# Kernel tuning notes

Measured on AMD Instinct MI355X. Metric: run time of the kernel, lower is better.

Reference implementation:

```python
import jax, jax.numpy as jnp
import numpy as np

B, S, D, H = 2, 2048, 4096, 16
HD = D // H          # 256 head dim
ROT = 64             # rotary_dim
MASK_FILL = -65504.0 # fp16 min, as in the IPEX kernel


def _sinusoidal_positions(num_pos, dim):
    inv_freq = 1.0 / (10000.0 ** (np.arange(0, dim, 2, dtype=np.float32) / dim))
    sinusoid = np.einsum('i,j->ij', np.arange(num_pos, dtype=np.float32), inv_freq)
    return np.concatenate([np.sin(sinusoid), np.cos(sinusoid)], axis=-1).astype(np.float32)  # [num_pos, dim]


def setup_inputs() -> dict:
    key = jax.random.key(0)
    ks = jax.random.split(key, 6)
    w = 0.02
    return {
        'hidden_states': jax.random.normal(ks[0], (B, S, D), jnp.float32),
        'Wq': jax.random.normal(ks[1], (D, D), jnp.float32) * w,
        'Wk': jax.random.normal(ks[2], (D, D), jnp.float32) * w,
        'Wv': jax.random.normal(ks[3], (D, D), jnp.float32) * w,
        'Wo': jax.random.normal(ks[4], (D, D), jnp.float32) * w,
        'embed_positions': jnp.asarray(_sinusoidal_positions(S, ROT)),  # [max_pos, ROT] sin|cos
        'attention_mask': jnp.zeros((B, 1, 1, S), jnp.float32),
        'position_ids': jnp.tile(jnp.arange(S, dtype=jnp.int32), (B, 1)),
    }


def rotate_every_two(x):
    x1 = x[..., ::2]
    x2 = x[..., 1::2]
    return jnp.stack((-x2, x1), axis=-1).reshape(x.shape)


def reference(hidden_states, Wq, Wk, Wv, Wo, embed_positions, attention_mask, position_ids):
    b, s, d = hidden_states.shape
    q = (hidden_states @ Wq).reshape(b, s, H, HD)
    k = (hidden_states @ Wk).reshape(b, s, H, HD)
    v = (hidden_states @ Wv).reshape(b, s, H, HD)

    # gather sin/cos per position, GPT-J interleaved layout
    sincos = embed_positions[position_ids]            # [b, s, ROT]
    sin, cos = jnp.split(sincos, 2, axis=-1)          # each [b, s, ROT/2]
    sin = jnp.repeat(sin, 2, axis=-1)[:, :, None, :]  # [b, s, 1, ROT]
    cos = jnp.repeat(cos, 2, axis=-1)[:, :, None, :]

    def rope(t):
        tr = t[..., :ROT]
        tr = tr * cos + rotate_every_two(tr) * sin
        return jnp.concatenate([tr, t[..., ROT:]], axis=-1)

    q = rope(q).transpose(0, 2, 1, 3)  # [b, H, s, HD]
    k = rope(k).transpose(0, 2, 1, 3)
    v = v.transpose(0, 2, 1, 3)

    scores = jnp.einsum('bhqd,bhkd->bhqk', q, k)
    causal = jnp.tril(jnp.ones((s, s), bool))
    # IPEX order: mask-fill with -65504 BEFORE dividing by sqrt(head_dim)
    scores = jnp.where(causal, scores, MASK_FILL) / jnp.sqrt(jnp.float32(HD))
    scores = scores + attention_mask
    attn = jax.nn.softmax(scores, axis=-1)

    out = jnp.einsum('bhqk,bhkd->bhqd', attn, v)
    out = out.transpose(0, 2, 1, 3).reshape(b, s, d)
    return out @ Wo
```

## Files before the change

kernel.cpp:

```cpp
#include <hip/hip_runtime.h>

typedef __bf16 bf16x8 __attribute__((ext_vector_type(8)));
typedef float f32x4 __attribute__((ext_vector_type(4)));
typedef unsigned short u16;
typedef unsigned int u32;
typedef u16 u16x8 __attribute__((ext_vector_type(8)));
typedef u16 u16x4 __attribute__((ext_vector_type(4)));

#define DEVI __device__ __forceinline__

static constexpr size_t R_ELEMS = (size_t)4096 * 4096;

DEVI u16 f2bf(float f) {
  u32 x = __float_as_uint(f);
  u32 r = x + 0x7FFFu + ((x >> 16) & 1u);
  return (u16)(r >> 16);
}
DEVI float bf2f(u16 u) { return __uint_as_float(((u32)u) << 16); }

#define GLOAD_LDS16(gp, lp)                                                     \
  __builtin_amdgcn_global_load_lds(                                             \
      (const __attribute__((address_space(1))) void*)(gp),                      \
      (__attribute__((address_space(3))) void*)(lp), 16, 0, 0)

__global__ void k_cvt(const float* __restrict__ in, u16* __restrict__ out, int n8) {
  int i = blockIdx.x * blockDim.x + threadIdx.x;
  if (i >= n8) return;
  const float4* p = (const float4*)in + (size_t)i * 2;
  float4 a = p[0], b = p[1];
  u16x8 o;
  o[0] = f2bf(a.x); o[1] = f2bf(a.y); o[2] = f2bf(a.z); o[3] = f2bf(a.w);
  o[4] = f2bf(b.x); o[5] = f2bf(b.y); o[6] = f2bf(b.z); o[7] = f2bf(b.w);
  *((u16x8*)out + i) = o;
}

__global__ void k_transpose_w(const float* __restrict__ W, u16* __restrict__ Wt) {
  __shared__ float t[64][65];
  int kb = blockIdx.x * 64, nb = blockIdx.y * 64;
  int tx = threadIdx.x, ty = threadIdx.y;
#pragma unroll
  for (int i = 0; i < 16; i++) {
    int r = i * 4 + ty;
    t[r][tx] = W[(size_t)(kb + r) * 4096 + nb + tx];
  }
  __syncthreads();
#pragma unroll
  for (int i = 0; i < 16; i++) {
    int r = i * 4 + ty;
    Wt[(size_t)(nb + r) * 4096 + kb + tx] = f2bf(t[tx][r]);
  }
}

__global__ void k_transpose_v(const u16* __restrict__ V, u16* __restrict__ Vt) {
  __shared__ u16 t[64][65];
  int s0 = blockIdx.x * 64, d0 = blockIdx.y * 64;
  size_t base = (size_t)blockIdx.z * (2048 * 256);
  int tx = threadIdx.x, ty = threadIdx.y;
#pragma unroll
  for (int i = 0; i < 16; i++) {
    int r = i * 4 + ty;
    t[r][tx] = V[base + (size_t)(s0 + r) * 256 + d0 + tx];
  }
  __syncthreads();
#pragma unroll
  for (int i = 0; i < 16; i++) {
    int r = i * 4 + ty;
    Vt[base + (size_t)(d0 + r) * 2048 + s0 + tx] = t[tx][r];
  }
}

__global__ void k_rope(u16* __restrict__ q, u16* __restrict__ k,
                       const float* __restrict__ ep, const int* __restrict__ pid) {
  int gid = blockIdx.x * blockDim.x + threadIdx.x;
  int pair = gid & 31;
  int row = gid >> 5;
  u16* base = (row < 65536) ? q : k;
  int rr = row & 65535;
  int b = rr >> 15;
  int s = rr & 2047;
  int pos = pid[b * 2048 + s];
  float sn = ep[pos * 64 + pair];
  float cs = ep[pos * 64 + 32 + pair];
  u16* p = base + (size_t)rr * 256 + pair * 2;
  float x0 = bf2f(p[0]), x1 = bf2f(p[1]);
  p[0] = f2bf(x0 * cs - x1 * sn);
  p[1] = f2bf(x1 * cs + x0 * sn);
}

template <int OUTMODE>
__global__ __launch_bounds__(256, 2) void k_gemm(const u16* __restrict__ A,
                                                 const u16* __restrict__ Bt,
                                                 void* __restrict__ outp) {
  __shared__ __attribute__((aligned(16))) u16 lA[128 * 64];
  __shared__ __attribute__((aligned(16))) u16 lB[128 * 64];
  const int tid = threadIdx.x;
  const int w = tid >> 6, lane = tid & 63;
  const int wr = w >> 1, wc = w & 1;
  const int m0 = blockIdx.y * 128, n0 = blockIdx.x * 128;

  f32x4 acc[4][4];
#pragma unroll
  for (int i = 0; i < 4; i++)
#pragma unroll
    for (int j = 0; j < 4; j++) acc[i][j] = (f32x4){0.f, 0.f, 0.f, 0.f};

  const int srow = lane >> 3;
  const int scol = ((lane & 7) ^ srow) * 8;
  const u16* Abase = A + (size_t)(m0 + w * 32 + srow) * 4096 + scol;
  const u16* Bbase = Bt + (size_t)(n0 + w * 32 + srow) * 4096 + scol;
  u16* lAw = lA + w * 2048;
  u16* lBw = lB + w * 2048;

  const int lm = lane & 15;
  const int lk = lane >> 4;
  const int swz = (lane & 7) << 3;

  for (int kt = 0; kt < 64; ++kt) {
    __syncthreads();
#pragma unroll
    for (int i = 0; i < 4; ++i) {
      GLOAD_LDS16(Abase + (size_t)kt * 64 + (size_t)i * 8 * 4096, lAw + i * 512);
      GLOAD_LDS16(Bbase + (size_t)kt * 64 + (size_t)i * 8 * 4096, lBw + i * 512);
    }
    __syncthreads();
#pragma unroll
    for (int ks = 0; ks < 2; ++ks) {
      bf16x8 af[4], bfr[4];
      const int ce = (ks * 32 + lk * 8) ^ swz;
#pragma unroll
      for (int mi = 0; mi < 4; mi++)
        af[mi] = *(const bf16x8*)(lA + (wr * 64 + mi * 16 + lm) * 64 + ce);
#pragma unroll
      for (int ni = 0; ni < 4; ni++)
        bfr[ni] = *(const bf16x8*)(lB + (wc * 64 + ni * 16 + lm) * 64 + ce);
#pragma unroll
      for (int mi = 0; mi < 4; mi++)
#pragma unroll
        for (int ni = 0; ni < 4; ni++)
          acc[mi][ni] = __builtin_amdgcn_mfma_f32_16x16x32_bf16(af[mi], bfr[ni],
                                                                acc[mi][ni], 0, 0, 0);
    }
  }

#pragma unroll
  for (int mi = 0; mi < 4; mi++) {
#pragma unroll
    for (int ni = 0; ni < 4; ni++) {
#pragma unroll
      for (int r = 0; r < 4; r++) {
        int m = m0 + wr * 64 + mi * 16 + lk * 4 + r;
        int n = n0 + wc * 64 + ni * 16 + lm;
        float v = acc[mi][ni][r];
        if (OUTMODE == 0) {
          u16* o = (u16*)outp;
          o[(size_t)((m >> 11) * 16 + (n >> 8)) * 524288 + (size_t)(m & 2047) * 256 +
            (n & 255)] = f2bf(v);
        } else {
          float* o = (float*)outp;
          o[(size_t)m * 4096 + n] = v;
        }
      }
    }
  }
}

__global__ __launch_bounds__(512, 2) void k_attn(const u16* __restrict__ Q,
                                                 const u16* __restrict__ K,
                                                 const u16* __restrict__ Vt,
                                                 const float* __restrict__ amask,
                                                 u16* __restrict__ AO) {
  __shared__ __attribute__((aligned(16))) u16 lK[2][64 * 256];
  __shared__ __attribute__((aligned(16))) u16 lV[2][256 * 64];
  __shared__ __attribute__((aligned(16))) u16 lP[8][16 * 64];

  const int tid = threadIdx.x, w = tid >> 6, lane = tid & 63;
  const int wg = blockIdx.x;
  const int bh = wg & 31;
  const int qt = (wg < 256) ? (15 - (wg >> 5)) : ((wg - 256) >> 5);
  const int b = bh >> 4;
  const int lm = lane & 15, lk = lane >> 4;
  const size_t head = (size_t)bh * (2048 * 256);
  const int q0 = qt * 128 + w * 16;
  const int swzl = (lane & 7) << 3;

  const int kreg_row = (lane >> 5);
  const int kcol = (lane & 31) * 8;
  const int vreg_row = (lane >> 3);
  const int vcol = (lane & 7) * 8;

#define ASTAGE(t)                                                                \
  {                                                                              \
    const int bb_ = (t) & 1;                                                     \
    const int kv0_ = (t) * 64;                                                   \
    _Pragma("unroll") for (int i_ = 0; i_ < 4; i_++) {                           \
      const int reg_ = w + i_ * 8;                                               \
      const int krow_ = reg_ * 2 + kreg_row;                                     \
      GLOAD_LDS16(K + head + (size_t)(kv0_ + krow_) * 256 +                      \
                      (kcol ^ ((krow_ & 7) << 3)),                               \
                  &lK[bb_][reg_ * 512 + lane * 8]);                              \
      const int vrow_ = reg_ * 8 + vreg_row;                                     \
      GLOAD_LDS16(Vt + head + (size_t)vrow_ * 2048 + kv0_ +                      \
                      (vcol ^ ((vrow_ & 7) << 3)),                               \
                  &lV[bb_][reg_ * 512 + lane * 8]);                              \
    }                                                                            \
  }

  bf16x8 qf[8];
#pragma unroll
  for (int c = 0; c < 8; c++)
    qf[c] = *(const bf16x8*)(Q + head + (size_t)(q0 + lm) * 256 + c * 32 + lk * 8);

  f32x4 o[16];
#pragma unroll
  for (int i = 0; i < 16; i++) o[i] = (f32x4){0.f, 0.f, 0.f, 0.f};
  float m_s = -__builtin_inff();
  float l_s = 0.f;

  const int ntiles = 2 * qt + 2;
  ASTAGE(0);

  for (int t = 0; t < ntiles; ++t) {
    const int kv0 = t * 64;
    const int bb = t & 1;
    float4 amq[4];
#pragma unroll
    for (int kb = 0; kb < 4; kb++)
      amq[kb] = *(const float4*)(amask + b * 2048 + kv0 + kb * 16 + lk * 4);
    if (t + 1 < ntiles) {
      ASTAGE(t + 1);
      asm volatile("s_waitcnt vmcnt(8)" ::: "memory");
    } else {
      asm volatile("s_waitcnt vmcnt(0)" ::: "memory");
    }
    __builtin_amdgcn_s_barrier();

    if (q0 + 15 >= kv0) {
      const u16* lKb = lK[bb];
      const u16* lVb = lV[bb];

      float sx[4][4];
      __builtin_amdgcn_s_setprio(1);
#pragma unroll
      for (int kb = 0; kb < 4; kb++) {
        f32x4 sa = (f32x4){0.f, 0.f, 0.f, 0.f};
        const int kvr = kb * 16 + lm;
#pragma unroll
        for (int c = 0; c < 8; c++) {
          bf16x8 kf = *(const bf16x8*)(lKb + kvr * 256 + ((c * 32 + lk * 8) ^ swzl));
          sa = __builtin_amdgcn_mfma_f32_16x16x32_bf16(kf, qf[c], sa, 0, 0, 0);
        }
#pragma unroll
        for (int r = 0; r < 4; r++)
          sx[kb][r] = sa[r] * 0.0625f + ((const float*)&amq[kb])[r];
      }
      __builtin_amdgcn_s_setprio(0);

      const int q_abs = q0 + lm;
      float tm = -__builtin_inff();
#pragma unroll
      for (int kb = 0; kb < 4; kb++)
#pragma unroll
        for (int r = 0; r < 4; r++) {
          bool valid = (kv0 + kb * 16 + lk * 4 + r) <= q_abs;
          tm = fmaxf(tm, valid ? sx[kb][r] : -__builtin_inff());
        }
      tm = fmaxf(tm, __shfl_xor(tm, 16, 64));
      tm = fmaxf(tm, __shfl_xor(tm, 32, 64));

      if (!__all(tm <= m_s + 8.0f)) {
        float mnew = fmaxf(m_s, tm);
        float alpha = __expf(m_s - mnew);
        m_s = mnew;
        l_s *= alpha;
        float af0 = __shfl(alpha, lk * 4 + 0, 64);
        float af1 = __shfl(alpha, lk * 4 + 1, 64);
        float af2 = __shfl(alpha, lk * 4 + 2, 64);
        float af3 = __shfl(alpha, lk * 4 + 3, 64);
#pragma unroll
        for (int dblk = 0; dblk < 16; dblk++) {
          o[dblk][0] *= af0; o[dblk][1] *= af1;
          o[dblk][2] *= af2; o[dblk][3] *= af3;
        }
      }

      float psum = 0.f;
#pragma unroll
      for (int kb = 0; kb < 4; kb++) {
        u16x4 ph;
#pragma unroll
        for (int r = 0; r < 4; r++) {
          bool valid = (kv0 + kb * 16 + lk * 4 + r) <= q_abs;
          float p = valid ? __expf(sx[kb][r] - m_s) : 0.f;
          psum += p;
          ph[r] = f2bf(p);
        }
        *(u16x4*)(&lP[w][lm * 64 + ((kb * 16 + lk * 4) ^ swzl)]) = ph;
      }
      psum += __shfl_xor(psum, 16, 64);
      psum += __shfl_xor(psum, 32, 64);
      l_s += psum;

      bf16x8 pa[2];
#pragma unroll
      for (int kh = 0; kh < 2; kh++)
        pa[kh] = *(const bf16x8*)(&lP[w][lm * 64 + ((lk * 8 + kh * 32) ^ swzl)]);
      __builtin_amdgcn_s_setprio(1);
#pragma unroll
      for (int dblk = 0; dblk < 16; dblk++) {
        const int dr = dblk * 16 + lm;
#pragma unroll
        for (int kh = 0; kh < 2; kh++) {
          bf16x8 vf = *(const bf16x8*)(lVb + dr * 64 + ((lk * 8 + kh * 32) ^ swzl));
          o[dblk] = __builtin_amdgcn_mfma_f32_16x16x32_bf16(pa[kh], vf, o[dblk], 0, 0, 0);
        }
      }
      __builtin_amdgcn_s_setprio(0);
    }
    __builtin_amdgcn_s_barrier();
  }
#undef ASTAGE

  float linv[4];
#pragma unroll
  for (int r = 0; r < 4; r++) linv[r] = 1.0f / __shfl(l_s, lk * 4 + r, 64);
#pragma unroll
  for (int r = 0; r < 4; r++) {
    const int s_abs = q0 + lk * 4 + r;
#pragma unroll
    for (int dblk = 0; dblk < 16; dblk++) {
      int d = (bh & 15) * 256 + dblk * 16 + lm;
      AO[((size_t)b * 2048 + s_abs) * 4096 + d] = f2bf(o[dblk][r] * linv[r]);
    }
  }
}

extern "C" void kernel_launch(void* const* d_in, const int* in_sizes, int n_in,
                              void* d_out, int out_size, void* d_ws, size_t ws_size,
                              hipStream_t stream) {
  (void)in_sizes; (void)n_in; (void)out_size; (void)ws_size;
  const float* hs = (const float*)d_in[0];
  const float* Wq = (const float*)d_in[1];
  const float* Wk = (const float*)d_in[2];
  const float* Wv = (const float*)d_in[3];
  const float* Wo = (const float*)d_in[4];
  const float* ep = (const float*)d_in[5];
  const float* am = (const float*)d_in[6];
  const int* pid = (const int*)d_in[7];

  u16* r0 = (u16*)d_ws;
  u16* r1 = r0 + R_ELEMS;
  u16* r2 = r1 + R_ELEMS;
  u16* r3 = r2 + R_ELEMS;
  u16* r4 = r3 + R_ELEMS;
  float* out = (float*)d_out;

  dim3 b256(256), b512(512), bT(64, 4);
  k_cvt<<<dim3(8192), b256, 0, stream>>>(hs, r0, 16777216 / 8);

  k_transpose_w<<<dim3(64, 64), bT, 0, stream>>>(Wq, r1);
  k_gemm<0><<<dim3(32, 32), b256, 0, stream>>>(r0, r1, r2);
  k_transpose_w<<<dim3(64, 64), bT, 0, stream>>>(Wk, r1);
  k_gemm<0><<<dim3(32, 32), b256, 0, stream>>>(r0, r1, r3);
  k_transpose_w<<<dim3(64, 64), bT, 0, stream>>>(Wv, r1);
  k_gemm<0><<<dim3(32, 32), b256, 0, stream>>>(r0, r1, r4);

  k_rope<<<dim3(16384), b256, 0, stream>>>(r2, r3, ep, pid);
  k_transpose_v<<<dim3(32, 4, 32), bT, 0, stream>>>(r4, r0);

  k_attn<<<dim3(512), b512, 0, stream>>>(r2, r3, r0, am, r4);

  k_transpose_w<<<dim3(64, 64), bT, 0, stream>>>(Wo, r1);
  k_gemm<1><<<dim3(32, 32), b256, 0, stream>>>(r4, r1, out);
}
```

Measured before the change: 776.3 us.

## Rewrite GEMM as 256x256 tile, 8-wave, double-buffered LDS pipeline with XCD remap

The bf16 GEMM goes from a 128x128 tile with 4 waves and a single LDS buffer to a 256x256 tile with 8 waves. Global-to-LDS loads are double-buffered and interleaved into four MFMA phases, using explicit vmcnt waits, barriers and setprio. Block IDs are remapped so neighbouring tiles land on the same XCD for better L2 reuse. The aim is to hide load latency behind MFMA work and raise data reuse, at the cost of 128KB of LDS, more registers, and a grid of only 256 blocks, which gives one wave of work with possible tail imbalance.

```diff
diff --git a/kernel.cpp b/kernel.cpp
--- a/kernel.cpp
+++ b/kernel.cpp
@@ -22,6 +22,8 @@
   __builtin_amdgcn_global_load_lds(                                             \
       (const __attribute__((address_space(1))) void*)(gp),                      \
       (__attribute__((address_space(3))) void*)(lp), 16, 0, 0)
+
+#define MFMA16(a, b, c) __builtin_amdgcn_mfma_f32_16x16x32_bf16((a), (b), (c), 0, 0, 0)
 
 __global__ void k_cvt(const float* __restrict__ in, u16* __restrict__ out, int n8) {
   int i = blockIdx.x * blockDim.x + threadIdx.x;
@@ -88,68 +90,148 @@
 }
 
 template <int OUTMODE>
-__global__ __launch_bounds__(256, 2) void k_gemm(const u16* __restrict__ A,
+__global__ __launch_bounds__(512, 2) void k_gemm(const u16* __restrict__ A,
                                                  const u16* __restrict__ Bt,
                                                  void* __restrict__ outp) {
-  __shared__ __attribute__((aligned(16))) u16 lA[128 * 64];
-  __shared__ __attribute__((aligned(16))) u16 lB[128 * 64];
+  __shared__ __attribute__((aligned(16))) u16 lA[2][256 * 64];
+  __shared__ __attribute__((aligned(16))) u16 lB[2][256 * 64];
   const int tid = threadIdx.x;
-  const int w = tid >> 6, lane = tid & 63;
-  const int wr = w >> 1, wc = w & 1;
-  const int m0 = blockIdx.y * 128, n0 = blockIdx.x * 128;
-
-  f32x4 acc[4][4];
-#pragma unroll
-  for (int i = 0; i < 4; i++)
+  const int w = tid >> 6, l = tid & 63;
+  const int wm = w >> 2, wn = w & 3;
+  const int bid = blockIdx.x;
+  const int wg = (bid & 7) * 32 + (bid >> 3);
+  const int m0 = (wg >> 4) * 256, n0 = (wg & 15) * 256;
+
+  const int lm = l & 15, lk = l >> 4;
+  const int co0 = (lk ^ (l & 7)) * 8;
+  const int co1 = ((4 + lk) ^ (l & 7)) * 8;
+
+  const int srow = w * 16 + (l >> 3);
+  const int scol = ((l & 7) ^ ((l >> 3) & 7)) * 8;
+  const int ldoff = w * 1024 + l * 8;
+
+  f32x4 acc[8][4];
+#pragma unroll
+  for (int i = 0; i < 8; i++)
 #pragma unroll
     for (int j = 0; j < 4; j++) acc[i][j] = (f32x4){0.f, 0.f, 0.f, 0.f};
 
-  const int srow = lane >> 3;
-  const int scol = ((lane & 7) ^ srow) * 8;
-  const u16* Abase = A + (size_t)(m0 + w * 32 + srow) * 4096 + scol;
-  const u16* Bbase = Bt + (size_t)(n0 + w * 32 + srow) * 4096 + scol;
-  u16* lAw = lA + w * 2048;
-  u16* lBw = lB + w * 2048;
-
-  const int lm = lane & 15;
-  const int lk = lane >> 4;
-  const int swz = (lane & 7) << 3;
-
-  for (int kt = 0; kt < 64; ++kt) {
-    __syncthreads();
-#pragma unroll
-    for (int i = 0; i < 4; ++i) {
-      GLOAD_LDS16(Abase + (size_t)kt * 64 + (size_t)i * 8 * 4096, lAw + i * 512);
-      GLOAD_LDS16(Bbase + (size_t)kt * 64 + (size_t)i * 8 * 4096, lBw + i * 512);
-    }
-    __syncthreads();
-#pragma unroll
-    for (int ks = 0; ks < 2; ++ks) {
-      bf16x8 af[4], bfr[4];
-      const int ce = (ks * 32 + lk * 8) ^ swz;
-#pragma unroll
-      for (int mi = 0; mi < 4; mi++)
-        af[mi] = *(const bf16x8*)(lA + (wr * 64 + mi * 16 + lm) * 64 + ce);
-#pragma unroll
-      for (int ni = 0; ni < 4; ni++)
-        bfr[ni] = *(const bf16x8*)(lB + (wc * 64 + ni * 16 + lm) * 64 + ce);
-#pragma unroll
-      for (int mi = 0; mi < 4; mi++)
-#pragma unroll
-        for (int ni = 0; ni < 4; ni++)
-          acc[mi][ni] = __builtin_amdgcn_mfma_f32_16x16x32_bf16(af[mi], bfr[ni],
-                                                                acc[mi][ni], 0, 0, 0);
-    }
-  }
-
-#pragma unroll
-  for (int mi = 0; mi < 4; mi++) {
+  auto stage_ht = [&](int h) {
+    if (h >= 256) return;
+    const int kt = h >> 2;
+    const int slot = h & 3;
+    const int rowbase = (slot >> 1) << 7;
+    const size_t gcol = (size_t)kt * 64 + scol;
+    if (slot & 1) {
+      const u16* g = A + (size_t)(m0 + rowbase + srow) * 4096 + gcol;
+      u16* d = &lA[kt & 1][rowbase * 64 + ldoff];
+      GLOAD_LDS16(g, d);
+      GLOAD_LDS16(g + 8 * 4096, d + 512);
+    } else {
+      const u16* g = Bt + (size_t)(n0 + rowbase + srow) * 4096 + gcol;
+      u16* d = &lB[kt & 1][rowbase * 64 + ldoff];
+      GLOAD_LDS16(g, d);
+      GLOAD_LDS16(g + 8 * 4096, d + 512);
+    }
+  };
+
+  for (int h = 0; h < 6; ++h) stage_ht(h);
+  asm volatile("s_waitcnt vmcnt(4)" ::: "memory");
+  __builtin_amdgcn_s_barrier();
+
+  bf16x8 af[4][2], bl[2][2], bh[2][2];
+
+  for (int t = 0; t < 64; ++t) {
+    const int hb = 4 * t + 6;
+    const u16* pA = &lA[t & 1][(wm * 128 + lm) * 64];
+    const u16* pB = &lB[t & 1][(wn * 64 + lm) * 64];
+
+#pragma unroll
+    for (int mi = 0; mi < 4; ++mi) {
+      af[mi][0] = *(const bf16x8*)(pA + mi * 1024 + co0);
+      af[mi][1] = *(const bf16x8*)(pA + mi * 1024 + co1);
+    }
+#pragma unroll
+    for (int ni = 0; ni < 2; ++ni) {
+      bl[ni][0] = *(const bf16x8*)(pB + ni * 1024 + co0);
+      bl[ni][1] = *(const bf16x8*)(pB + ni * 1024 + co1);
+    }
+    stage_ht(hb);
+    __builtin_amdgcn_s_barrier();
+    __builtin_amdgcn_s_setprio(1);
+#pragma unroll
+    for (int mi = 0; mi < 4; ++mi)
+#pragma unroll
+      for (int ni = 0; ni < 2; ++ni) {
+        acc[mi][ni] = MFMA16(af[mi][0], bl[ni][0], acc[mi][ni]);
+        acc[mi][ni] = MFMA16(af[mi][1], bl[ni][1], acc[mi][ni]);
+      }
+    __builtin_amdgcn_s_setprio(0);
+    __builtin_amdgcn_s_barrier();
+
+#pragma unroll
+    for (int ni = 0; ni < 2; ++ni) {
+      bh[ni][0] = *(const bf16x8*)(pB + (2 + ni) * 1024 + co0);
+      bh[ni][1] = *(const bf16x8*)(pB + (2 + ni) * 1024 + co1);
+    }
+    stage_ht(hb + 1);
+    __builtin_amdgcn_s_barrier();
+    __builtin_amdgcn_s_setprio(1);
+#pragma unroll
+    for (int mi = 0; mi < 4; ++mi)
+#pragma unroll
+      for (int ni = 0; ni < 2; ++ni) {
+        acc[mi][2 + ni] = MFMA16(af[mi][0], bh[ni][0], acc[mi][2 + ni]);
+        acc[mi][2 + ni] = MFMA16(af[mi][1], bh[ni][1], acc[mi][2 + ni]);
+      }
+    __builtin_amdgcn_s_setprio(0);
+    __builtin_amdgcn_s_barrier();
+
+#pragma unroll
+    for (int mi = 0; mi < 4; ++mi) {
+      af[mi][0] = *(const bf16x8*)(pA + (4 + mi) * 1024 + co0);
+      af[mi][1] = *(const bf16x8*)(pA + (4 + mi) * 1024 + co1);
+    }
+    stage_ht(hb + 2);
+    __builtin_amdgcn_s_barrier();
+    __builtin_amdgcn_s_setprio(1);
+#pragma unroll
+    for (int mi = 0; mi < 4; ++mi)
+#pragma unroll
+      for (int ni = 0; ni < 2; ++ni) {
+        acc[4 + mi][2 + ni] = MFMA16(af[mi][0], bh[ni][0], acc[4 + mi][2 + ni]);
+        acc[4 + mi][2 + ni] = MFMA16(af[mi][1], bh[ni][1], acc[4 + mi][2 + ni]);
+      }
+    __builtin_amdgcn_s_setprio(0);
+    __builtin_amdgcn_s_barrier();
+
+    stage_ht(hb + 3);
+    if (t < 62) {
+      asm volatile("s_waitcnt vmcnt(4)" ::: "memory");
+    } else {
+      asm volatile("s_waitcnt vmcnt(0)" ::: "memory");
+    }
+    __builtin_amdgcn_s_barrier();
+    __builtin_amdgcn_s_setprio(1);
+#pragma unroll
+    for (int mi = 0; mi < 4; ++mi)
+#pragma unroll
+      for (int ni = 0; ni < 2; ++ni) {
+        acc[4 + mi][ni] = MFMA16(af[mi][0], bl[ni][0], acc[4 + mi][ni]);
+        acc[4 + mi][ni] = MFMA16(af[mi][1], bl[ni][1], acc[4 + mi][ni]);
+      }
+    __builtin_amdgcn_s_setprio(0);
+    __builtin_amdgcn_s_barrier();
+  }
+
+#pragma unroll
+  for (int mi = 0; mi < 8; mi++) {
 #pragma unroll
     for (int ni = 0; ni < 4; ni++) {
 #pragma unroll
       for (int r = 0; r < 4; r++) {
-        int m = m0 + wr * 64 + mi * 16 + lk * 4 + r;
-        int n = n0 + wc * 64 + ni * 16 + lm;
+        int m = m0 + wm * 128 + mi * 16 + lk * 4 + r;
+        int n = n0 + wn * 64 + ni * 16 + lm;
         float v = acc[mi][ni][r];
         if (OUTMODE == 0) {
           u16* o = (u16*)outp;
@@ -358,11 +440,11 @@
   k_cvt<<<dim3(8192), b256, 0, stream>>>(hs, r0, 16777216 / 8);
 
   k_transpose_w<<<dim3(64, 64), bT, 0, stream>>>(Wq, r1);
-  k_gemm<0><<<dim3(32, 32), b256, 0, stream>>>(r0, r1, r2);
+  k_gemm<0><<<dim3(256), b512, 0, stream>>>(r0, r1, r2);
   k_transpose_w<<<dim3(64, 64), bT, 0, stream>>>(Wk, r1);
-  k_gemm<0><<<dim3(32, 32), b256, 0, stream>>>(r0, r1, r3);
+  k_gemm<0><<<dim3(256), b512, 0, stream>>>(r0, r1, r3);
   k_transpose_w<<<dim3(64, 64), bT, 0, stream>>>(Wv, r1);
-  k_gemm<0><<<dim3(32, 32), b256, 0, stream>>>(r0, r1, r4);
+  k_gemm<0><<<dim3(256), b512, 0, stream>>>(r0, r1, r4);
 
   k_rope<<<dim3(16384), b256, 0, stream>>>(r2, r3, ep, pid);
   k_transpose_v<<<dim3(32, 4, 32), bT, 0, stream>>>(r4, r0);
@@ -370,5 +452,5 @@
   k_attn<<<dim3(512), b512, 0, stream>>>(r2, r3, r0, am, r4);
 
   k_transpose_w<<<dim3(64, 64), bT, 0, stream>>>(Wo, r1);
-  k_gemm<1><<<dim3(32, 32), b256, 0, stream>>>(r4, r1, out);
-}
+  k_gemm<1><<<dim3(256), b512, 0, stream>>>(r4, r1, out);
+}
```

Result: no change. 783.1 us (+0.9%).

## Fuse Q and K projection GEMMs into one kernel sharing A tiles

Applied to the files above, without the earlier changes.

Adds a k_gemm_qk kernel that computes the Q and K projections together, loading each activation tile into LDS once and multiplying it against both weight tiles. The activation matrix is read from global memory once instead of twice, and one GEMM launch is removed. In exchange each block keeps two accumulator sets (128 fp32 values per lane) and uses 48KB of LDS, which may cause register spills or lower occupancy under launch_bounds(256,2). Workspace buffers are reassigned so that Wk gets its own transposed buffer.

```diff
diff --git a/kernel.cpp b/kernel.cpp
--- a/kernel.cpp
+++ b/kernel.cpp
@@ -22,6 +22,8 @@
   __builtin_amdgcn_global_load_lds(                                             \
       (const __attribute__((address_space(1))) void*)(gp),                      \
       (__attribute__((address_space(3))) void*)(lp), 16, 0, 0)
+
+#define MFMA16(a, b, c) __builtin_amdgcn_mfma_f32_16x16x32_bf16((a), (b), (c), 0, 0, 0)
 
 __global__ void k_cvt(const float* __restrict__ in, u16* __restrict__ out, int n8) {
   int i = blockIdx.x * blockDim.x + threadIdx.x;
@@ -137,8 +139,7 @@
       for (int mi = 0; mi < 4; mi++)
 #pragma unroll
         for (int ni = 0; ni < 4; ni++)
-          acc[mi][ni] = __builtin_amdgcn_mfma_f32_16x16x32_bf16(af[mi], bfr[ni],
-                                                                acc[mi][ni], 0, 0, 0);
+          acc[mi][ni] = MFMA16(af[mi], bfr[ni], acc[mi][ni]);
     }
   }
 
@@ -159,6 +160,93 @@
           float* o = (float*)outp;
           o[(size_t)m * 4096 + n] = v;
         }
+      }
+    }
+  }
+}
+
+__global__ __launch_bounds__(256, 2) void k_gemm_qk(const u16* __restrict__ A,
+                                                    const u16* __restrict__ Btq,
+                                                    const u16* __restrict__ Btk,
+                                                    u16* __restrict__ Qo,
+                                                    u16* __restrict__ Ko) {
+  __shared__ __attribute__((aligned(16))) u16 lA[128 * 64];
+  __shared__ __attribute__((aligned(16))) u16 lBq[128 * 64];
+  __shared__ __attribute__((aligned(16))) u16 lBk[128 * 64];
+  const int tid = threadIdx.x;
+  const int w = tid >> 6, lane = tid & 63;
+  const int wr = w >> 1, wc = w & 1;
+  const int m0 = blockIdx.y * 128, n0 = blockIdx.x * 128;
+
+  f32x4 accq[4][4], acck[4][4];
+#pragma unroll
+  for (int i = 0; i < 4; i++)
+#pragma unroll
+    for (int j = 0; j < 4; j++) {
+      accq[i][j] = (f32x4){0.f, 0.f, 0.f, 0.f};
+      acck[i][j] = (f32x4){0.f, 0.f, 0.f, 0.f};
+    }
+
+  const int srow = lane >> 3;
+  const int scol = ((lane & 7) ^ srow) * 8;
+  const u16* Abase = A + (size_t)(m0 + w * 32 + srow) * 4096 + scol;
+  const u16* Bqb = Btq + (size_t)(n0 + w * 32 + srow) * 4096 + scol;
+  const u16* Bkb = Btk + (size_t)(n0 + w * 32 + srow) * 4096 + scol;
+  u16* lAw = lA + w * 2048;
+  u16* lBqw = lBq + w * 2048;
+  u16* lBkw = lBk + w * 2048;
+
+  const int lm = lane & 15;
+  const int lk = lane >> 4;
+  const int swz = (lane & 7) << 3;
+
+  for (int kt = 0; kt < 64; ++kt) {
+    __syncthreads();
+#pragma unroll
+    for (int i = 0; i < 4; ++i) {
+      GLOAD_LDS16(Abase + (size_t)kt * 64 + (size_t)i * 8 * 4096, lAw + i * 512);
+      GLOAD_LDS16(Bqb + (size_t)kt * 64 + (size_t)i * 8 * 4096, lBqw + i * 512);
+      GLOAD_LDS16(Bkb + (size_t)kt * 64 + (size_t)i * 8 * 4096, lBkw + i * 512);
+    }
+    __syncthreads();
+#pragma unroll
+    for (int ks = 0; ks < 2; ++ks) {
+      bf16x8 af[4], bfr[4];
+      const int ce = (ks * 32 + lk * 8) ^ swz;
+#pragma unroll
+      for (int mi = 0; mi < 4; mi++)
+        af[mi] = *(const bf16x8*)(lA + (wr * 64 + mi * 16 + lm) * 64 + ce);
+#pragma unroll
+      for (int ni = 0; ni < 4; ni++)
+        bfr[ni] = *(const bf16x8*)(lBq + (wc * 64 + ni * 16 + lm) * 64 + ce);
+#pragma unroll
+      for (int mi = 0; mi < 4; mi++)
+#pragma unroll
+        for (int ni = 0; ni < 4; ni++)
+          accq[mi][ni] = MFMA16(af[mi], bfr[ni], accq[mi][ni]);
+#pragma unroll
+      for (int ni = 0; ni < 4; ni++)
+        bfr[ni] = *(const bf16x8*)(lBk + (wc * 64 + ni * 16 + lm) * 64 + ce);
+#pragma unroll
+      for (int mi = 0; mi < 4; mi++)
+#pragma unroll
+        for (int ni = 0; ni < 4; ni++)
+          acck[mi][ni] = MFMA16(af[mi], bfr[ni], acck[mi][ni]);
+    }
+  }
+
+#pragma unroll
+  for (int mi = 0; mi < 4; mi++) {
+#pragma unroll
+    for (int ni = 0; ni < 4; ni++) {
+#pragma unroll
+      for (int r = 0; r < 4; r++) {
+        int m = m0 + wr * 64 + mi * 16 + lk * 4 + r;
+        int n = n0 + wc * 64 + ni * 16 + lm;
+        size_t idx = (size_t)((m >> 11) * 16 + (n >> 8)) * 524288 +
+                     (size_t)(m & 2047) * 256 + (n & 255);
+        Qo[idx] = f2bf(accq[mi][ni][r]);
+        Ko[idx] = f2bf(acck[mi][ni][r]);
       }
     }
   }
@@ -358,17 +446,17 @@
   k_cvt<<<dim3(8192), b256, 0, stream>>>(hs, r0, 16777216 / 8);
 
   k_transpose_w<<<dim3(64, 64), bT, 0, stream>>>(Wq, r1);
+  k_transpose_w<<<dim3(64, 64), bT, 0, stream>>>(Wk, r2);
+  k_gemm_qk<<<dim3(32, 32), b256, 0, stream>>>(r0, r1, r2, r3, r4);
+
+  k_transpose_w<<<dim3(64, 64), bT, 0, stream>>>(Wv, r1);
   k_gemm<0><<<dim3(32, 32), b256, 0, stream>>>(r0, r1, r2);
-  k_transpose_w<<<dim3(64, 64), bT, 0, stream>>>(Wk, r1);
-  k_gemm<0><<<dim3(32, 32), b256, 0, stream>>>(r0, r1, r3);
-  k_transpose_w<<<dim3(64, 64), bT, 0, stream>>>(Wv, r1);
-  k_gemm<0><<<dim3(32, 32), b256, 0, stream>>>(r0, r1, r4);
-
-  k_rope<<<dim3(16384), b256, 0, stream>>>(r2, r3, ep, pid);
-  k_transpose_v<<<dim3(32, 4, 32), bT, 0, stream>>>(r4, r0);
-
-  k_attn<<<dim3(512), b512, 0, stream>>>(r2, r3, r0, am, r4);
+
+  k_rope<<<dim3(16384), b256, 0, stream>>>(r3, r4, ep, pid);
+  k_transpose_v<<<dim3(32, 4, 32), bT, 0, stream>>>(r2, r0);
+
+  k_attn<<<dim3(512), b512, 0, stream>>>(r3, r4, r0, am, r2);
 
   k_transpose_w<<<dim3(64, 64), bT, 0, stream>>>(Wo, r1);
-  k_gemm<1><<<dim3(32, 32), b256, 0, stream>>>(r4, r1, out);
-}
+  k_gemm<1><<<dim3(32, 32), b256, 0, stream>>>(r2, r1, out);
+}
```

New measurement: 750.7 us. 1.03x faster.
